# Kernel optimization log

Measured on AMD Instinct MI355X. Metric: run time of the kernel, lower is better.

The kernel has to match this reference:

```python
import jax, jax.numpy as jnp
import numpy as np

V, E, B, NODES_PER_GRAPH = 100000, 128, 4096, 64
N = B * NODES_PER_GRAPH  # 262144 nodes per side
EPS = 1e-6


def setup_inputs() -> dict:
    key = jax.random.key(0)
    k1, k2, k3, k4, k5, k6 = jax.random.split(key, 6)
    left_x = jax.random.randint(k1, (N, 1), 0, V, dtype=jnp.int64 if jax.config.jax_enable_x64 else jnp.int32)
    right_x = jax.random.randint(k2, (N, 1), 0, V, dtype=left_x.dtype)
    # sorted segment ids with every graph non-empty (64 nodes per graph)
    batch_ids = jnp.repeat(jnp.arange(B, dtype=left_x.dtype), NODES_PER_GRAPH)
    label = jax.random.randint(k3, (B,), 0, 2).astype(jnp.float32)
    emb_table = jax.random.normal(k4, (V, E), dtype=jnp.float32)
    W = jax.random.normal(k5, (E, E), dtype=jnp.float32) / np.sqrt(E)
    b = jax.random.normal(k6, (E,), dtype=jnp.float32) * 0.01
    return {
        "left_x": left_x,
        "left_graph_index": jnp.arange(B, dtype=left_x.dtype),
        "right_x": right_x,
        "right_graph_index": jnp.arange(B, dtype=left_x.dtype),
        "left_x_batch": batch_ids,
        "right_x_batch": batch_ids,
        "label": label,
        "emb_table": emb_table,
        "W": W,
        "b": b,
    }


def _side_emb(x, x_batch, emb_table, W, b, num_segments):
    node_emb = emb_table[x[:, 0]]                       # [N, E] gather
    pooled = jax.ops.segment_max(node_emb, x_batch,      # [B, E] scatter-max
                                 num_segments=num_segments,
                                 indices_are_sorted=True)
    return pooled @ W.T + b                              # trans_linear


def reference(left_x, left_graph_index, right_x, right_graph_index,
              left_x_batch, right_x_batch, label, emb_table, W, b):
    num_segments = label.shape[0]
    left_final = _side_emb(left_x, left_x_batch, emb_table, W, b, num_segments)
    right_final = _side_emb(right_x, right_x_batch, emb_table, W, b, num_segments)
    # torch CosineSimilarity(eps=1e-6): clamp each norm at eps
    dot = jnp.sum(left_final * right_final, axis=-1)
    nl = jnp.maximum(jnp.linalg.norm(left_final, axis=-1), EPS)
    nr = jnp.maximum(jnp.linalg.norm(right_final, axis=-1), EPS)
    cos = dot / (nl * nr)                                # [B]
    # ContrastiveLoss(margin=1.0), size_average=True
    losses = 0.5 * ((1.0 - label) * cos ** 2
                    + label * jnp.maximum(1.0 - cos, 0.0) ** 2)
    sim_loss = losses.mean()
    return sim_loss, cos
```

## Files before the change

kernel.cpp:

```cpp
#include <hip/hip_runtime.h>
#include <math.h>

#define B_GRAPHS 4096
#define NPG 64
#define E_DIM 128
#define INV_B (1.0f / 4096.0f)

static __device__ __forceinline__ float4 fmax4(float4 a, float4 b) {
    return make_float4(fmaxf(a.x, b.x), fmaxf(a.y, b.y),
                       fmaxf(a.z, b.z), fmaxf(a.w, b.w));
}

__global__ __launch_bounds__(256) void gather_pool_k(
    const int* __restrict__ lx, const int* __restrict__ rx,
    const float* __restrict__ emb, float* __restrict__ pooled)
{
    const int g    = blockIdx.x;
    const int side = blockIdx.y;
    const int t    = threadIdx.x;
    const int w    = t >> 6;
    const int lane = t & 63;

    __shared__ int   idx[NPG];
    __shared__ float red[4][E_DIM];

    const int* __restrict__ x = side ? rx : lx;
    if (t < NPG) idx[t] = x[g * NPG + t];
    __syncthreads();

    const int n0 = t >> 5;
    const int q  = t & 31;
    const float4* __restrict__ e4 = reinterpret_cast<const float4*>(emb);

    float4 a = make_float4(-INFINITY, -INFINITY, -INFINITY, -INFINITY);
    #pragma unroll
    for (int i = 0; i < 8; ++i)
        a = fmax4(a, e4[(size_t)idx[(i << 3) + n0] * 32 + q]);

    a.x = fmaxf(a.x, __shfl_xor(a.x, 32));
    a.y = fmaxf(a.y, __shfl_xor(a.y, 32));
    a.z = fmaxf(a.z, __shfl_xor(a.z, 32));
    a.w = fmaxf(a.w, __shfl_xor(a.w, 32));

    if (lane < 32) {
        const int o = w * 32 + lane;
        red[0][o] = a.x; red[1][o] = a.y; red[2][o] = a.z; red[3][o] = a.w;
    }
    __syncthreads();

    if (t < 32) {
        float4 m;
        m.x = fmaxf(fmaxf(red[0][t],      red[0][32 + t]),
                    fmaxf(red[0][64 + t], red[0][96 + t]));
        m.y = fmaxf(fmaxf(red[1][t],      red[1][32 + t]),
                    fmaxf(red[1][64 + t], red[1][96 + t]));
        m.z = fmaxf(fmaxf(red[2][t],      red[2][32 + t]),
                    fmaxf(red[2][64 + t], red[2][96 + t]));
        m.w = fmaxf(fmaxf(red[3][t],      red[3][32 + t]),
                    fmaxf(red[3][64 + t], red[3][96 + t]));
        reinterpret_cast<float4*>(pooled)[((size_t)side * B_GRAPHS + g) * 32 + t] = m;
    }
}

__global__ __launch_bounds__(256) void matvec_cos_k(
    const float* __restrict__ pooled, const float* __restrict__ W,
    const float* __restrict__ bias, const float* __restrict__ label,
    float* __restrict__ out)
{
    const int g    = blockIdx.x;
    const int t    = threadIdx.x;
    const int w    = t >> 6;
    const int lane = t & 63;

    __shared__ float4 P4[2][32];
    __shared__ float  wred[3][4];

    if (t < 64) {
        const int side = t >> 5;
        const int qq   = t & 31;
        P4[side][qq] = reinterpret_cast<const float4*>(pooled)
            [((size_t)side * B_GRAPHS + g) * 32 + qq];
    }
    __syncthreads();

    float acc;
    {
        const int side = t & 1;
        const int e    = t >> 1;
        acc = bias[e];
        const float4* __restrict__ wr =
            reinterpret_cast<const float4*>(W) + (size_t)e * 32;
        const float4* __restrict__ pv = P4[side];
        #pragma unroll 8
        for (int fi = 0; fi < 32; ++fi) {
            const float4 wv = wr[fi];
            const float4 p  = pv[fi];
            acc = fmaf(p.x, wv.x, acc);
            acc = fmaf(p.y, wv.y, acc);
            acc = fmaf(p.z, wv.z, acc);
            acc = fmaf(p.w, wv.w, acc);
        }
    }

    {
        const float other = __shfl_xor(acc, 1);
        const float l = (t & 1) ? other : acc;
        const float r = (t & 1) ? acc   : other;
        float dot = l * r;
        float nl  = l * l;
        float nr  = r * r;
        #pragma unroll
        for (int off = 1; off < 64; off <<= 1) {
            dot += __shfl_xor(dot, off);
            nl  += __shfl_xor(nl,  off);
            nr  += __shfl_xor(nr,  off);
        }
        if (lane == 0) {
            wred[0][w] = dot; wred[1][w] = nl; wred[2][w] = nr;
        }
    }
    __syncthreads();

    if (t == 0) {
        const float dd = 0.5f * (wred[0][0] + wred[0][1] + wred[0][2] + wred[0][3]);
        const float ll = 0.5f * (wred[1][0] + wred[1][1] + wred[1][2] + wred[1][3]);
        const float rr = 0.5f * (wred[2][0] + wred[2][1] + wred[2][2] + wred[2][3]);
        const float nlv = fmaxf(sqrtf(ll), 1e-6f);
        const float nrv = fmaxf(sqrtf(rr), 1e-6f);
        const float c   = dd / (nlv * nrv);
        out[1 + g] = c;
        const float lab  = label[g];
        const float mm   = fmaxf(1.0f - c, 0.0f);
        const float loss = 0.5f * ((1.0f - lab) * c * c + lab * mm * mm);
        atomicAdd(out, loss * INV_B);
    }
}

extern "C" void kernel_launch(void* const* d_in, const int* in_sizes, int n_in,
                              void* d_out, int out_size, void* d_ws, size_t ws_size,
                              hipStream_t stream)
{
    const int*   lx    = (const int*)d_in[0];
    const int*   rx    = (const int*)d_in[2];
    const float* label = (const float*)d_in[6];
    const float* emb   = (const float*)d_in[7];
    const float* W     = (const float*)d_in[8];
    const float* bias  = (const float*)d_in[9];

    float* out    = (float*)d_out;
    float* pooled = (float*)d_ws;

    hipMemsetAsync(out, 0, sizeof(float), stream);

    dim3 gA(B_GRAPHS, 2);
    gather_pool_k<<<gA, 256, 0, stream>>>(lx, rx, emb, pooled);
    matvec_cos_k<<<B_GRAPHS, 256, 0, stream>>>(pooled, W, bias, label, out);
}
```

Baseline: 191.4 us.

## Batch eight graphs per block in matvec and stage W in shared memory

The matvec/cosine kernel now processes 8 graphs per block. It loads W into padded LDS in two 64-row halves and reuses it across all 8 graphs and both sides. This cuts the repeated per-graph global/L2 reads of the full weight matrix. The per-block reduction is replaced by one wave per graph computing the cosine directly. In exchange it uses more LDS per block, launches fewer blocks, and adds extra syncs.

```diff
diff --git a/kernel.cpp b/kernel.cpp
--- a/kernel.cpp
+++ b/kernel.cpp
@@ -5,6 +5,8 @@
 #define NPG 64
 #define E_DIM 128
 #define INV_B (1.0f / 4096.0f)
+#define GPB 8
+#define LDSW 129
 
 static __device__ __forceinline__ float4 fmax4(float4 a, float4 b) {
     return make_float4(fmaxf(a.x, b.x), fmaxf(a.y, b.y),
@@ -67,48 +69,63 @@
     const float* __restrict__ bias, const float* __restrict__ label,
     float* __restrict__ out)
 {
-    const int g    = blockIdx.x;
+    __shared__ float Wl[64 * LDSW];
+    __shared__ float P[GPB][2][E_DIM];
+
     const int t    = threadIdx.x;
+    const int g0   = blockIdx.x * GPB;
     const int w    = t >> 6;
     const int lane = t & 63;
 
-    __shared__ float4 P4[2][32];
-    __shared__ float  wred[3][4];
+    for (int i = t; i < GPB * 2 * E_DIM / 4; i += 256) {
+        const int word = i * 4;
+        const int g = word >> 8, s = (word >> 7) & 1, f = word & 127;
+        const float4 v = reinterpret_cast<const float4*>(pooled)
+            [(((size_t)s * B_GRAPHS + g0 + g) * E_DIM + f) >> 2];
+        float* dst = &P[g][s][f];
+        dst[0] = v.x; dst[1] = v.y; dst[2] = v.z; dst[3] = v.w;
+    }
 
-    if (t < 64) {
-        const int side = t >> 5;
-        const int qq   = t & 31;
-        P4[side][qq] = reinterpret_cast<const float4*>(pooled)
-            [((size_t)side * B_GRAPHS + g) * 32 + qq];
-    }
-    __syncthreads();
+    float fin[2][2][2];
 
-    float acc;
-    {
-        const int side = t & 1;
-        const int e    = t >> 1;
-        acc = bias[e];
-        const float4* __restrict__ wr =
-            reinterpret_cast<const float4*>(W) + (size_t)e * 32;
-        const float4* __restrict__ pv = P4[side];
-        #pragma unroll 8
-        for (int fi = 0; fi < 32; ++fi) {
-            const float4 wv = wr[fi];
-            const float4 p  = pv[fi];
-            acc = fmaf(p.x, wv.x, acc);
-            acc = fmaf(p.y, wv.y, acc);
-            acc = fmaf(p.z, wv.z, acc);
-            acc = fmaf(p.w, wv.w, acc);
+    #pragma unroll
+    for (int h = 0; h < 2; ++h) {
+        __syncthreads();
+        for (int i = t; i < 64 * E_DIM / 4; i += 256) {
+            const int word = i * 4;
+            const int row = word >> 7, col = word & 127;
+            const float4 v = reinterpret_cast<const float4*>(W)
+                [((h * 64 + row) * E_DIM + col) >> 2];
+            float* dst = &Wl[row * LDSW + col];
+            dst[0] = v.x; dst[1] = v.y; dst[2] = v.z; dst[3] = v.w;
+        }
+        __syncthreads();
+
+        const float be = bias[h * 64 + lane];
+        const float* __restrict__ wr = &Wl[lane * LDSW];
+        #pragma unroll
+        for (int gi = 0; gi < 2; ++gi) {
+            const int gg = gi * 4 + w;
+            const float* __restrict__ p0 = &P[gg][0][0];
+            const float* __restrict__ p1 = &P[gg][1][0];
+            float fa = be, fb = be;
+            #pragma unroll 8
+            for (int f = 0; f < E_DIM; ++f) {
+                const float wv = wr[f];
+                fa = fmaf(p0[f], wv, fa);
+                fb = fmaf(p1[f], wv, fb);
+            }
+            fin[gi][h][0] = fa;
+            fin[gi][h][1] = fb;
         }
     }
 
-    {
-        const float other = __shfl_xor(acc, 1);
-        const float l = (t & 1) ? other : acc;
-        const float r = (t & 1) ? acc   : other;
-        float dot = l * r;
-        float nl  = l * l;
-        float nr  = r * r;
+    #pragma unroll
+    for (int gi = 0; gi < 2; ++gi) {
+        const int gg = gi * 4 + w;
+        float dot = fin[gi][0][0] * fin[gi][0][1] + fin[gi][1][0] * fin[gi][1][1];
+        float nl  = fin[gi][0][0] * fin[gi][0][0] + fin[gi][1][0] * fin[gi][1][0];
+        float nr  = fin[gi][0][1] * fin[gi][0][1] + fin[gi][1][1] * fin[gi][1][1];
         #pragma unroll
         for (int off = 1; off < 64; off <<= 1) {
             dot += __shfl_xor(dot, off);
@@ -116,23 +133,16 @@
             nr  += __shfl_xor(nr,  off);
         }
         if (lane == 0) {
-            wred[0][w] = dot; wred[1][w] = nl; wred[2][w] = nr;
+            const int g = g0 + gg;
+            const float nlv = fmaxf(sqrtf(nl), 1e-6f);
+            const float nrv = fmaxf(sqrtf(nr), 1e-6f);
+            const float c   = dot / (nlv * nrv);
+            out[1 + g] = c;
+            const float lab  = label[g];
+            const float mm   = fmaxf(1.0f - c, 0.0f);
+            const float loss = 0.5f * ((1.0f - lab) * c * c + lab * mm * mm);
+            atomicAdd(out, loss * INV_B);
         }
-    }
-    __syncthreads();
-
-    if (t == 0) {
-        const float dd = 0.5f * (wred[0][0] + wred[0][1] + wred[0][2] + wred[0][3]);
-        const float ll = 0.5f * (wred[1][0] + wred[1][1] + wred[1][2] + wred[1][3]);
-        const float rr = 0.5f * (wred[2][0] + wred[2][1] + wred[2][2] + wred[2][3]);
-        const float nlv = fmaxf(sqrtf(ll), 1e-6f);
-        const float nrv = fmaxf(sqrtf(rr), 1e-6f);
-        const float c   = dd / (nlv * nrv);
-        out[1 + g] = c;
-        const float lab  = label[g];
-        const float mm   = fmaxf(1.0f - c, 0.0f);
-        const float loss = 0.5f * ((1.0f - lab) * c * c + lab * mm * mm);
-        atomicAdd(out, loss * INV_B);
     }
 }
 
@@ -154,5 +164,5 @@
 
     dim3 gA(B_GRAPHS, 2);
     gather_pool_k<<<gA, 256, 0, stream>>>(lx, rx, emb, pooled);
-    matvec_cos_k<<<B_GRAPHS, 256, 0, stream>>>(pooled, W, bias, label, out);
+    matvec_cos_k<<<B_GRAPHS / GPB, 256, 0, stream>>>(pooled, W, bias, label, out);
 }
```

New measurement: 196.4 us. 2.6% more time.
